# Kernel optimization log

Hardware: AMD Instinct MI355X
Metric: run time of the kernel (lower is better)

Reference implementation:

```python
import jax, jax.numpy as jnp
import numpy as np

N, E, G = 50000, 800000, 128
IN_C, H, EDGE_D, NUM_CLASSES, NUM_LAYERS = 26, 64, 3, 2, 4

def _p(k, shape):
    return jax.random.normal(k, shape, dtype=jnp.float32) * 0.05

def setup_inputs() -> dict:
    key = jax.random.key(0)
    ks = list(jax.random.split(key, 32))
    x = jax.random.normal(ks[0], (N, IN_C), dtype=jnp.float32)
    pos = jax.random.normal(ks[1], (N, 3), dtype=jnp.float32)
    row = jax.random.randint(ks[2], (E,), 0, N, dtype=jnp.int32)
    # avoid self-loops so dist > 0 (norm is non-differentiable at 0)
    off = jax.random.randint(ks[3], (E,), 1, N, dtype=jnp.int32)
    col = (row + off) % N
    edge_index = jnp.stack([row, col], axis=0)
    edge_attr = jax.random.normal(ks[4], (E, EDGE_D), dtype=jnp.float32)
    batch = jnp.sort(jax.random.randint(ks[5], (N,), 0, G, dtype=jnp.int32))
    inp = dict(x=x, pos=pos, edge_index=edge_index, edge_attr=edge_attr, batch=batch)
    inp['proj_W'] = _p(ks[6], (IN_C, H)); inp['proj_b'] = jnp.zeros((H,), jnp.float32)
    inp['msg_W1'] = _p(ks[7], (NUM_LAYERS, 2*H + 1 + EDGE_D, H)); inp['msg_b1'] = jnp.zeros((NUM_LAYERS, H), jnp.float32)
    inp['msg_W2'] = _p(ks[8], (NUM_LAYERS, H, H)); inp['msg_b2'] = jnp.zeros((NUM_LAYERS, H), jnp.float32)
    inp['node_W1'] = _p(ks[9], (NUM_LAYERS, 2*H, H)); inp['node_b1'] = jnp.zeros((NUM_LAYERS, H), jnp.float32)
    inp['node_W2'] = _p(ks[10], (NUM_LAYERS, H, H)); inp['node_b2'] = jnp.zeros((NUM_LAYERS, H), jnp.float32)
    inp['coord_W1'] = _p(ks[11], (NUM_LAYERS - 1, H, H)); inp['coord_b1'] = jnp.zeros((NUM_LAYERS - 1, H), jnp.float32)
    inp['coord_W2'] = _p(ks[12], (NUM_LAYERS - 1, H, 1)); inp['coord_b2'] = jnp.zeros((NUM_LAYERS - 1, 1), jnp.float32)
    inp['cls_W1'] = _p(ks[13], (2*H, H)); inp['cls_b1'] = jnp.zeros((H,), jnp.float32)
    inp['cls_W2'] = _p(ks[14], (H, NUM_CLASSES)); inp['cls_b2'] = jnp.zeros((NUM_CLASSES,), jnp.float32)
    return inp

def _egnn_forward(x, pos, edge_index, edge_attr, batch,
                  proj_W, proj_b, msg_W1, msg_b1, msg_W2, msg_b2,
                  node_W1, node_b1, node_W2, node_b2,
                  coord_W1, coord_b1, coord_W2, coord_b2,
                  cls_W1, cls_b1, cls_W2, cls_b2):
    silu = jax.nn.silu
    row, col = edge_index[0], edge_index[1]
    h = x @ proj_W + proj_b  # [N,H]
    for i in range(NUM_LAYERS):
        diff = pos[row] - pos[col]                      # [E,3]
        dist = jnp.linalg.norm(diff, axis=-1, keepdims=True)  # [E,1]
        msg_in = jnp.concatenate([h[row], h[col], dist, edge_attr], axis=-1)  # [E,2H+1+edge_dim]
        msg = silu(silu(msg_in @ msg_W1[i] + msg_b1[i]) @ msg_W2[i] + msg_b2[i])  # [E,H]
        agg = jax.ops.segment_sum(msg, row, num_segments=N)  # [N,H]
        h_new = silu(jnp.concatenate([h, agg], axis=-1) @ node_W1[i] + node_b1[i]) @ node_W2[i] + node_b2[i]
        h = h + h_new  # residual; dropout is identity at eval
        if i < NUM_LAYERS - 1:
            w = silu(msg @ coord_W1[i] + coord_b1[i]) @ coord_W2[i] + coord_b2[i]  # [E,1]
            pos = pos + jax.ops.segment_sum(diff * w, row, num_segments=N)
    # mean_max pooling over graphs
    sums = jax.ops.segment_sum(h, batch, num_segments=G)
    counts = jax.ops.segment_sum(jnp.ones((h.shape[0],), h.dtype), batch, num_segments=G)
    mean = sums / jnp.maximum(counts, 1.0)[:, None]
    mx = jax.ops.segment_max(h, batch, num_segments=G)
    pooled = jnp.concatenate([mean, mx], axis=-1)  # [G,2H]
    return jax.nn.relu(pooled @ cls_W1 + cls_b1) @ cls_W2 + cls_b2  # [G,num_classes]

def reference(x, pos, edge_index, edge_attr, batch,
              proj_W, proj_b, msg_W1, msg_b1, msg_W2, msg_b2,
              node_W1, node_b1, node_W2, node_b2,
              coord_W1, coord_b1, coord_W2, coord_b2,
              cls_W1, cls_b1, cls_W2, cls_b2):
    return _egnn_forward(x, pos, edge_index, edge_attr, batch,
                         proj_W, proj_b, msg_W1, msg_b1, msg_W2, msg_b2,
                         node_W1, node_b1, node_W2, node_b2,
                         coord_W1, coord_b1, coord_W2, coord_b2,
                         cls_W1, cls_b1, cls_W2, cls_b2)
```

## Files before the change

### kernel.cpp

```cpp
#include <hip/hip_runtime.h>
#include <math.h>


typedef __attribute__((ext_vector_type(8))) short bshort8;
typedef __attribute__((ext_vector_type(4))) float f32x4;
typedef unsigned short ushort;
typedef unsigned int uint;

__device__ __forceinline__ float silu_f(float x)
{
  return x * __builtin_amdgcn_rcpf(1.0f + __expf(-x));
}

__device__ __forceinline__ void bf16_split(float x, ushort& h, ushort& l)
{
  uint bx = __float_as_uint(x);
  ushort hb = (ushort)(bx >> 16);
  float hf = __uint_as_float((uint)hb << 16);
  float r = x - hf;
  l = (ushort)(__float_as_uint(r) >> 16);
  h = hb;
}

#define ROW_FMA(acc, scal, rowptr)                                                   \
  {                                                                                  \
    const float4* _w = (const float4*)(rowptr);                                      \
    _Pragma("unroll") for (int _j = 0; _j < 16; _j++)                                \
    {                                                                                \
      float4 _wv = _w[_j];                                                           \
      acc[4 * _j + 0] += (scal) * _wv.x;                                             \
      acc[4 * _j + 1] += (scal) * _wv.y;                                             \
      acc[4 * _j + 2] += (scal) * _wv.z;                                             \
      acc[4 * _j + 3] += (scal) * _wv.w;                                             \
    }                                                                                \
  }

__global__ __launch_bounds__(256) void proj_kernel(
    const float* __restrict__ x, const float* __restrict__ W, const float* __restrict__ b,
    float* __restrict__ h, int N)
{
  __shared__ float sW[26 * 64];
  __shared__ float sb[64];
  for (int i = threadIdx.x; i < 26 * 64; i += 256) sW[i] = W[i];
  if (threadIdx.x < 64) sb[threadIdx.x] = b[threadIdx.x];
  __syncthreads();
  int n = blockIdx.x * 256 + threadIdx.x;
  if (n >= N) return;
  float acc[64];
#pragma unroll
  for (int j = 0; j < 64; j++) acc[j] = sb[j];
#pragma unroll
  for (int k = 0; k < 26; k++) {
    float xk = x[(size_t)n * 26 + k];
    ROW_FMA(acc, xk, sW + k * 64);
  }
  float4* h4 = (float4*)(h + (size_t)n * 64);
#pragma unroll
  for (int j4 = 0; j4 < 16; j4++) {
    float4 v;
    v.x = acc[4 * j4 + 0]; v.y = acc[4 * j4 + 1]; v.z = acc[4 * j4 + 2]; v.w = acc[4 * j4 + 3];
    h4[j4] = v;
  }
}

#define NB 128
#define ASTR 132

__global__ __launch_bounds__(256) void premul_tiled_kernel(
    const float* __restrict__ h, const float* __restrict__ W1,
    float* __restrict__ P, float* __restrict__ Q, int N)
{
  __shared__ float sA[64 * ASTR];
  __shared__ float sW[64 * 64];
  int t = threadIdx.x;
  int n0 = blockIdx.x * NB;

#pragma unroll
  for (int it = 0; it < 8; it++) {
    int f = t + 256 * it;
    int nl = f >> 4;
    int k4 = f & 15;
    int n = n0 + nl;
    float4 v;
    if (n < N) v = ((const float4*)(h + (size_t)n * 64))[k4];
    else { v.x = v.y = v.z = v.w = 0.f; }
    sA[(4 * k4 + 0) * ASTR + nl] = v.x;
    sA[(4 * k4 + 1) * ASTR + nl] = v.y;
    sA[(4 * k4 + 2) * ASTR + nl] = v.z;
    sA[(4 * k4 + 3) * ASTR + nl] = v.w;
  }
  for (int i = t; i < 4096; i += 256) sW[i] = W1[i];
  __syncthreads();

  int rg = t & 31, cg = t >> 5;
  const float4* sA4 = (const float4*)sA;
  const float4* sW4 = (const float4*)sW;

  float aP[4][8];
#pragma unroll
  for (int i = 0; i < 4; i++)
#pragma unroll
    for (int j = 0; j < 8; j++) aP[i][j] = 0.f;
#pragma unroll 8
  for (int k = 0; k < 64; k++) {
    float4 a = sA4[k * (ASTR / 4) + rg];
    float4 w0 = sW4[k * 16 + 2 * cg];
    float4 w1 = sW4[k * 16 + 2 * cg + 1];
#pragma unroll
    for (int i = 0; i < 4; i++) {
      float av = (i == 0) ? a.x : (i == 1) ? a.y : (i == 2) ? a.z : a.w;
      aP[i][0] += av * w0.x; aP[i][1] += av * w0.y;
      aP[i][2] += av * w0.z; aP[i][3] += av * w0.w;
      aP[i][4] += av * w1.x; aP[i][5] += av * w1.y;
      aP[i][6] += av * w1.z; aP[i][7] += av * w1.w;
    }
  }
  __syncthreads();
  for (int i = t; i < 4096; i += 256) sW[i] = W1[4096 + i];
  __syncthreads();
  float aQ[4][8];
#pragma unroll
  for (int i = 0; i < 4; i++)
#pragma unroll
    for (int j = 0; j < 8; j++) aQ[i][j] = 0.f;
#pragma unroll 8
  for (int k = 0; k < 64; k++) {
    float4 a = sA4[k * (ASTR / 4) + rg];
    float4 w0 = sW4[k * 16 + 2 * cg];
    float4 w1 = sW4[k * 16 + 2 * cg + 1];
#pragma unroll
    for (int i = 0; i < 4; i++) {
      float av = (i == 0) ? a.x : (i == 1) ? a.y : (i == 2) ? a.z : a.w;
      aQ[i][0] += av * w0.x; aQ[i][1] += av * w0.y;
      aQ[i][2] += av * w0.z; aQ[i][3] += av * w0.w;
      aQ[i][4] += av * w1.x; aQ[i][5] += av * w1.y;
      aQ[i][6] += av * w1.z; aQ[i][7] += av * w1.w;
    }
  }
#pragma unroll
  for (int i = 0; i < 4; i++) {
    int n = n0 + 4 * rg + i;
    if (n < N) {
      float4 o0, o1;
      o0.x = aP[i][0]; o0.y = aP[i][1]; o0.z = aP[i][2]; o0.w = aP[i][3];
      o1.x = aP[i][4]; o1.y = aP[i][5]; o1.z = aP[i][6]; o1.w = aP[i][7];
      float4* Pp = (float4*)(P + (size_t)n * 64 + 8 * cg);
      Pp[0] = o0; Pp[1] = o1;
      o0.x = aQ[i][0]; o0.y = aQ[i][1]; o0.z = aQ[i][2]; o0.w = aQ[i][3];
      o1.x = aQ[i][4]; o1.y = aQ[i][5]; o1.z = aQ[i][6]; o1.w = aQ[i][7];
      float4* Qp = (float4*)(Q + (size_t)n * 64 + 8 * cg);
      Qp[0] = o0; Qp[1] = o1;
    }
  }
}

template <int PREMUL>
__global__ __launch_bounds__(256) void node_tiled_kernel(
    float* __restrict__ h, const float* __restrict__ agg,
    const float* __restrict__ W1, const float* __restrict__ b1,
    const float* __restrict__ W2, const float* __restrict__ b2, int N,
    const float* __restrict__ W1n, float* __restrict__ P, float* __restrict__ Q)
{
  __shared__ float sA[64 * ASTR];
  __shared__ float sW[64 * 64];
  __shared__ float sb1v[64], sb2v[64];
  int t = threadIdx.x;
  int n0 = blockIdx.x * NB;
  int rg = t & 31, cg = t >> 5;
  const float4* sA4 = (const float4*)sA;
  const float4* sW4 = (const float4*)sW;

#pragma unroll
  for (int it = 0; it < 8; it++) {
    int f = t + 256 * it;
    int nl = f >> 4;
    int k4 = f & 15;
    int n = n0 + nl;
    float4 v;
    if (n < N) v = ((const float4*)(h + (size_t)n * 64))[k4];
    else { v.x = v.y = v.z = v.w = 0.f; }
    sA[(4 * k4 + 0) * ASTR + nl] = v.x;
    sA[(4 * k4 + 1) * ASTR + nl] = v.y;
    sA[(4 * k4 + 2) * ASTR + nl] = v.z;
    sA[(4 * k4 + 3) * ASTR + nl] = v.w;
  }
  for (int i = t; i < 4096; i += 256) sW[i] = W1[i];
  if (t < 64) { sb1v[t] = b1[t]; sb2v[t] = b2[t]; }
  __syncthreads();

  float u[4][8];
#pragma unroll
  for (int i = 0; i < 4; i++)
#pragma unroll
    for (int j = 0; j < 8; j++) u[i][j] = 0.f;
#pragma unroll 8
  for (int k = 0; k < 64; k++) {
    float4 a = sA4[k * (ASTR / 4) + rg];
    float4 w0 = sW4[k * 16 + 2 * cg];
    float4 w1 = sW4[k * 16 + 2 * cg + 1];
#pragma unroll
    for (int i = 0; i < 4; i++) {
      float av = (i == 0) ? a.x : (i == 1) ? a.y : (i == 2) ? a.z : a.w;
      u[i][0] += av * w0.x; u[i][1] += av * w0.y;
      u[i][2] += av * w0.z; u[i][3] += av * w0.w;
      u[i][4] += av * w1.x; u[i][5] += av * w1.y;
      u[i][6] += av * w1.z; u[i][7] += av * w1.w;
    }
  }
  __syncthreads();

#pragma unroll
  for (int it = 0; it < 8; it++) {
    int f = t + 256 * it;
    int nl = f >> 4;
    int k4 = f & 15;
    int n = n0 + nl;
    float4 v;
    if (n < N) v = ((const float4*)(agg + (size_t)n * 64))[k4];
    else { v.x = v.y = v.z = v.w = 0.f; }
    sA[(4 * k4 + 0) * ASTR + nl] = v.x;
    sA[(4 * k4 + 1) * ASTR + nl] = v.y;
    sA[(4 * k4 + 2) * ASTR + nl] = v.z;
    sA[(4 * k4 + 3) * ASTR + nl] = v.w;
  }
  for (int i = t; i < 4096; i += 256) sW[i] = W1[4096 + i];
  __syncthreads();
#pragma unroll 8
  for (int k = 0; k < 64; k++) {
    float4 a = sA4[k * (ASTR / 4) + rg];
    float4 w0 = sW4[k * 16 + 2 * cg];
    float4 w1 = sW4[k * 16 + 2 * cg + 1];
#pragma unroll
    for (int i = 0; i < 4; i++) {
      float av = (i == 0) ? a.x : (i == 1) ? a.y : (i == 2) ? a.z : a.w;
      u[i][0] += av * w0.x; u[i][1] += av * w0.y;
      u[i][2] += av * w0.z; u[i][3] += av * w0.w;
      u[i][4] += av * w1.x; u[i][5] += av * w1.y;
      u[i][6] += av * w1.z; u[i][7] += av * w1.w;
    }
  }
#pragma unroll
  for (int i = 0; i < 4; i++)
#pragma unroll
    for (int j = 0; j < 8; j++) u[i][j] = silu_f(u[i][j] + sb1v[8 * cg + j]);
  __syncthreads();

#pragma unroll
  for (int j = 0; j < 8; j++)
#pragma unroll
    for (int i = 0; i < 4; i++) sA[(8 * cg + j) * ASTR + (4 * rg + i)] = u[i][j];
  for (int i = t; i < 4096; i += 256) sW[i] = W2[i];
  __syncthreads();

  float o[4][8];
#pragma unroll
  for (int i = 0; i < 4; i++)
#pragma unroll
    for (int j = 0; j < 8; j++) o[i][j] = 0.f;
#pragma unroll 8
  for (int k = 0; k < 64; k++) {
    float4 a = sA4[k * (ASTR / 4) + rg];
    float4 w0 = sW4[k * 16 + 2 * cg];
    float4 w1 = sW4[k * 16 + 2 * cg + 1];
#pragma unroll
    for (int i = 0; i < 4; i++) {
      float av = (i == 0) ? a.x : (i == 1) ? a.y : (i == 2) ? a.z : a.w;
      o[i][0] += av * w0.x; o[i][1] += av * w0.y;
      o[i][2] += av * w0.z; o[i][3] += av * w0.w;
      o[i][4] += av * w1.x; o[i][5] += av * w1.y;
      o[i][6] += av * w1.z; o[i][7] += av * w1.w;
    }
  }
  float hnew[4][8];
#pragma unroll
  for (int i = 0; i < 4; i++) {
    int n = n0 + 4 * rg + i;
    if (n < N) {
      float4* hp = (float4*)(h + (size_t)n * 64 + 8 * cg);
      float4 h0 = hp[0], h1 = hp[1];
      hnew[i][0] = h0.x + o[i][0] + sb2v[8 * cg + 0];
      hnew[i][1] = h0.y + o[i][1] + sb2v[8 * cg + 1];
      hnew[i][2] = h0.z + o[i][2] + sb2v[8 * cg + 2];
      hnew[i][3] = h0.w + o[i][3] + sb2v[8 * cg + 3];
      hnew[i][4] = h1.x + o[i][4] + sb2v[8 * cg + 4];
      hnew[i][5] = h1.y + o[i][5] + sb2v[8 * cg + 5];
      hnew[i][6] = h1.z + o[i][6] + sb2v[8 * cg + 6];
      hnew[i][7] = h1.w + o[i][7] + sb2v[8 * cg + 7];
      float4 s0, s1;
      s0.x = hnew[i][0]; s0.y = hnew[i][1]; s0.z = hnew[i][2]; s0.w = hnew[i][3];
      s1.x = hnew[i][4]; s1.y = hnew[i][5]; s1.z = hnew[i][6]; s1.w = hnew[i][7];
      hp[0] = s0; hp[1] = s1;
    } else {
#pragma unroll
      for (int j = 0; j < 8; j++) hnew[i][j] = 0.f;
    }
  }

  if (PREMUL) {
    __syncthreads();
#pragma unroll
    for (int j = 0; j < 8; j++)
#pragma unroll
      for (int i = 0; i < 4; i++) sA[(8 * cg + j) * ASTR + (4 * rg + i)] = hnew[i][j];
    for (int i = t; i < 4096; i += 256) sW[i] = W1n[i];
    __syncthreads();
    float aP[4][8];
#pragma unroll
    for (int i = 0; i < 4; i++)
#pragma unroll
      for (int j = 0; j < 8; j++) aP[i][j] = 0.f;
#pragma unroll 8
    for (int k = 0; k < 64; k++) {
      float4 a = sA4[k * (ASTR / 4) + rg];
      float4 w0 = sW4[k * 16 + 2 * cg];
      float4 w1 = sW4[k * 16 + 2 * cg + 1];
#pragma unroll
      for (int i = 0; i < 4; i++) {
        float av = (i == 0) ? a.x : (i == 1) ? a.y : (i == 2) ? a.z : a.w;
        aP[i][0] += av * w0.x; aP[i][1] += av * w0.y;
        aP[i][2] += av * w0.z; aP[i][3] += av * w0.w;
        aP[i][4] += av * w1.x; aP[i][5] += av * w1.y;
        aP[i][6] += av * w1.z; aP[i][7] += av * w1.w;
      }
    }
#pragma unroll
    for (int i = 0; i < 4; i++) {
      int n = n0 + 4 * rg + i;
      if (n < N) {
        float4 o0, o1;
        o0.x = aP[i][0]; o0.y = aP[i][1]; o0.z = aP[i][2]; o0.w = aP[i][3];
        o1.x = aP[i][4]; o1.y = aP[i][5]; o1.z = aP[i][6]; o1.w = aP[i][7];
        float4* Pp = (float4*)(P + (size_t)n * 64 + 8 * cg);
        Pp[0] = o0; Pp[1] = o1;
      }
    }
    __syncthreads();
    for (int i = t; i < 4096; i += 256) sW[i] = W1n[4096 + i];
    __syncthreads();
    float aQ[4][8];
#pragma unroll
    for (int i = 0; i < 4; i++)
#pragma unroll
      for (int j = 0; j < 8; j++) aQ[i][j] = 0.f;
#pragma unroll 8
    for (int k = 0; k < 64; k++) {
      float4 a = sA4[k * (ASTR / 4) + rg];
      float4 w0 = sW4[k * 16 + 2 * cg];
      float4 w1 = sW4[k * 16 + 2 * cg + 1];
#pragma unroll
      for (int i = 0; i < 4; i++) {
        float av = (i == 0) ? a.x : (i == 1) ? a.y : (i == 2) ? a.z : a.w;
        aQ[i][0] += av * w0.x; aQ[i][1] += av * w0.y;
        aQ[i][2] += av * w0.z; aQ[i][3] += av * w0.w;
        aQ[i][4] += av * w1.x; aQ[i][5] += av * w1.y;
        aQ[i][6] += av * w1.z; aQ[i][7] += av * w1.w;
      }
    }
#pragma unroll
    for (int i = 0; i < 4; i++) {
      int n = n0 + 4 * rg + i;
      if (n < N) {
        float4 o0, o1;
        o0.x = aQ[i][0]; o0.y = aQ[i][1]; o0.z = aQ[i][2]; o0.w = aQ[i][3];
        o1.x = aQ[i][4]; o1.y = aQ[i][5]; o1.z = aQ[i][6]; o1.w = aQ[i][7];
        float4* Qp = (float4*)(Q + (size_t)n * 64 + 8 * cg);
        Qp[0] = o0; Qp[1] = o1;
      }
    }
  }
}

__global__ __launch_bounds__(256) void hist_kernel(
    const int* __restrict__ row, int* __restrict__ cnt, int E)
{
  int e = blockIdx.x * 256 + threadIdx.x;
  if (e < E) atomicAdd(&cnt[row[e]], 1);
}

__global__ __launch_bounds__(1024) void scan_kernel(
    const int* __restrict__ cnt, int* __restrict__ rowptr, int* __restrict__ cursor, int N, int E)
{
  __shared__ int part[1024];
  int t = threadIdx.x;
  int chunk = (N + 1023) >> 10;
  int lo = t * chunk;
  int hi = lo + chunk;
  if (lo > N) lo = N;
  if (hi > N) hi = N;
  int s = 0;
  for (int i = lo; i < hi; i++) s += cnt[i];
  part[t] = s;
  __syncthreads();
  for (int off = 1; off < 1024; off <<= 1) {
    int v = 0;
    if (t >= off) v = part[t - off];
    __syncthreads();
    if (t >= off) part[t] += v;
    __syncthreads();
  }
  int run = part[t] - s;
  for (int i = lo; i < hi; i++) {
    rowptr[i] = run;
    cursor[i] = run;
    run += cnt[i];
  }
  if (t == 0) rowptr[N] = E;
}

__global__ __launch_bounds__(256) void scatter_kernel(
    const int* __restrict__ row, const int* __restrict__ col, const float* __restrict__ eattr,
    int* __restrict__ cursor, int* __restrict__ srow, int* __restrict__ scol,
    float* __restrict__ sea4, int E)
{
  int e = blockIdx.x * 256 + threadIdx.x;
  if (e >= E) return;
  int r = row[e];
  int p = atomicAdd(&cursor[r], 1);
  srow[p] = r;
  scol[p] = col[e];
  float4 v;
  v.x = eattr[(size_t)e * 3 + 0];
  v.y = eattr[(size_t)e * 3 + 1];
  v.z = eattr[(size_t)e * 3 + 2];
  v.w = 0.f;
  ((float4*)sea4)[p] = v;
}

__global__ __launch_bounds__(256) void prep_wt_kernel(
    const float* __restrict__ W2all, const float* __restrict__ C1all,
    ushort* __restrict__ w2h, ushort* __restrict__ w2l,
    ushort* __restrict__ c1h, ushort* __restrict__ c1l)
{
  int idx = blockIdx.x * 256 + threadIdx.x;
  if (idx >= 4 * 4096) return;
  int layer = idx >> 12, rem = idx & 4095;
  int k = rem >> 6, c = rem & 63;
  int oidx = layer * 4096 + c * 64 + k;
  ushort h, l;
  bf16_split(W2all[idx], h, l);
  w2h[oidx] = h; w2l[oidx] = l;
  if (layer < 3) {
    bf16_split(C1all[idx], h, l);
    c1h[oidx] = h; c1l[oidx] = l;
  }
}

#define EB 128

__device__ __forceinline__ bshort8 lds_frag(const ushort* base, int edge, int kb)
{
  int byte = edge * 128 + kb * 2;
  byte ^= (edge & 7) << 4;
  return *(const bshort8*)((const char*)base + byte);
}

template <int COORD>
__global__ __launch_bounds__(256) void edge_fused_kernel(
    const int* __restrict__ srow, const int* __restrict__ scol, const int* __restrict__ rowptr,
    const float* __restrict__ posr, float* __restrict__ posw,
    const float* __restrict__ sea4,
    const float* __restrict__ P, const float* __restrict__ Q,
    const float* __restrict__ W1t, const float* __restrict__ b1,
    const ushort* __restrict__ w2h, const ushort* __restrict__ w2l,
    const float* __restrict__ b2,
    const ushort* __restrict__ c1h, const ushort* __restrict__ c1l,
    const float* __restrict__ cb1, const float* __restrict__ cW2,
    const float* __restrict__ cb2,
    float* __restrict__ agg, int E)
{
  __shared__ ushort sUhi[EB * 64];
  __shared__ ushort sUlo[EB * 64];
  __shared__ float sW1t[4 * 64];
  __shared__ float sb1v[64], sb2v[64];
  __shared__ float sDiff[3][EB];
  __shared__ float sWe[EB];
  __shared__ int sShare[COORD ? EB * 4 : EB];
  __shared__ float scb1v[COORD ? 64 : 1];
  __shared__ float scW2v[COORD ? 64 : 1];
  __shared__ int sSlotCnt[2];
  __shared__ int sSlotStart[EB + 2];
  __shared__ int sSlotRowF[EB];

  int* s_srow = sShare;
  float* sPart = (float*)sShare;

  int t = threadIdx.x;
  sW1t[t] = W1t[t];
  if (t < 64) { sb1v[t] = b1[t]; sb2v[t] = b2[t]; }
  if (COORD && t >= 64 && t < 128) { scb1v[t - 64] = cb1[t - 64]; scW2v[t - 64] = cW2[t - 64]; }
  __syncthreads();

  int e0 = blockIdx.x * EB;
  int nE = E - e0; if (nE > EB) nE = EB;

#pragma unroll
  for (int p = 0; p < 4; p++) {
    int eloc = p * 32 + (t >> 3);
    int ks = t & 7;
    int e = e0 + eloc;
    int base = eloc * 128 + ks * 16;
    int swz = (eloc & 7) << 4;
    if (e < E) {
      int r = srow[e];
      int c = scol[e];
      float prx = posr[(size_t)r * 3 + 0], pry = posr[(size_t)r * 3 + 1],
            prz = posr[(size_t)r * 3 + 2];
      float pcx = posr[(size_t)c * 3 + 0], pcy = posr[(size_t)c * 3 + 1],
            pcz = posr[(size_t)c * 3 + 2];
      float dx = prx - pcx, dy = pry - pcy, dz = prz - pcz;
      float dist = sqrtf(dx * dx + dy * dy + dz * dz);
      if (ks == 0) {
        s_srow[eloc] = r;
        sDiff[0][eloc] = dx; sDiff[1][eloc] = dy; sDiff[2][eloc] = dz;
      }
      float4 ea = ((const float4*)sea4)[e];
      const float4* P4p = (const float4*)(P + (size_t)r * 64) + ks * 2;
      const float4* Q4p = (const float4*)(Q + (size_t)c * 64) + ks * 2;
      float4 a0 = P4p[0], a1 = P4p[1];
      float4 q0 = Q4p[0], q1 = Q4p[1];
      float pa[8] = {a0.x, a0.y, a0.z, a0.w, a1.x, a1.y, a1.z, a1.w};
      float qa[8] = {q0.x, q0.y, q0.z, q0.w, q1.x, q1.y, q1.z, q1.w};
      ushort hh[8], ll[8];
#pragma unroll
      for (int kk = 0; kk < 8; kk++) {
        int k = ks * 8 + kk;
        float val = pa[kk] + qa[kk] + sb1v[k] + dist * sW1t[k] + ea.x * sW1t[64 + k] +
                    ea.y * sW1t[128 + k] + ea.z * sW1t[192 + k];
        float uv = silu_f(val);
        bf16_split(uv, hh[kk], ll[kk]);
      }
      uint4 hv, lv;
      hv.x = (uint)hh[0] | ((uint)hh[1] << 16);
      hv.y = (uint)hh[2] | ((uint)hh[3] << 16);
      hv.z = (uint)hh[4] | ((uint)hh[5] << 16);
      hv.w = (uint)hh[6] | ((uint)hh[7] << 16);
      lv.x = (uint)ll[0] | ((uint)ll[1] << 16);
// ... 198 lines not shown
  ssum[grp][j] = s;
  smax[grp][j] = mx;
  __syncthreads();
  if (grp == 0) {
    float S = ssum[0][j] + ssum[1][j] + ssum[2][j] + ssum[3][j];
    float M = fmaxf(fmaxf(smax[0][j], smax[1][j]), fmaxf(smax[2][j], smax[3][j]));
    float cnt = (float)(end - start);
    pooled[j] = S / fmaxf(cnt, 1.0f);
    pooled[64 + j] = M;
  }
  __syncthreads();
  if (threadIdx.x < 64) {
    float a = b1[j];
#pragma unroll
    for (int k = 0; k < 128; k++) a += pooled[k] * W1[k * 64 + j];
    su[j] = fmaxf(a, 0.f);
  }
  __syncthreads();
  if (threadIdx.x < 2) {
    float a = b2[threadIdx.x];
#pragma unroll
    for (int k = 0; k < 64; k++) a += su[k] * W2[k * 2 + threadIdx.x];
    out[g * 2 + threadIdx.x] = a;
  }
}

extern "C" void kernel_launch(void* const* d_in, const int* in_sizes, int n_in,
                              void* d_out, int out_size, void* d_ws, size_t ws_size,
                              hipStream_t stream)
{
  const float* x = (const float*)d_in[0];
  const float* pos = (const float*)d_in[1];
  const int* ei = (const int*)d_in[2];
  const float* eattr = (const float*)d_in[3];
  const int* batch = (const int*)d_in[4];
  const float* projW = (const float*)d_in[5];
  const float* projb = (const float*)d_in[6];
  const float* msgW1 = (const float*)d_in[7];
  const float* msgb1 = (const float*)d_in[8];
  const float* msgW2 = (const float*)d_in[9];
  const float* msgb2 = (const float*)d_in[10];
  const float* ndW1 = (const float*)d_in[11];
  const float* ndb1 = (const float*)d_in[12];
  const float* ndW2 = (const float*)d_in[13];
  const float* ndb2 = (const float*)d_in[14];
  const float* cdW1 = (const float*)d_in[15];
  const float* cdb1 = (const float*)d_in[16];
  const float* cdW2 = (const float*)d_in[17];
  const float* cdb2 = (const float*)d_in[18];
  const float* clsW1 = (const float*)d_in[19];
  const float* clsb1 = (const float*)d_in[20];
  const float* clsW2 = (const float*)d_in[21];
  const float* clsb2 = (const float*)d_in[22];

  int N = in_sizes[4];
  int E = in_sizes[3] / 3;
  const int* rowp = ei;
  const int* colp = ei + E;

  char* wsb = (char*)d_ws;
  size_t off = 0;
  auto alloc = [&](size_t bytes) {
    size_t o = off;
    off = (off + bytes + 255) & ~(size_t)255;
    return o;
  };
  size_t nh = (size_t)N * 64 * sizeof(float);
  size_t o_h = alloc(nh);
  size_t o_P = alloc(nh);
  size_t o_Q = alloc(nh);
  size_t o_agg = alloc(nh);
  size_t o_posA = alloc((size_t)N * 3 * sizeof(float));
  size_t o_posB = alloc((size_t)N * 3 * sizeof(float));
  size_t o_cnt = alloc((size_t)N * sizeof(int));
  size_t o_rowptr = alloc(((size_t)N + 1) * sizeof(int));
  size_t o_cursor = alloc((size_t)N * sizeof(int));
  size_t o_srow = alloc((size_t)E * sizeof(int));
  size_t o_scol = alloc((size_t)E * sizeof(int));
  size_t o_sea4 = alloc((size_t)E * 4 * sizeof(float));
  size_t o_w2h = alloc(4 * 4096 * sizeof(ushort));
  size_t o_w2l = alloc(4 * 4096 * sizeof(ushort));
  size_t o_c1h = alloc(4 * 4096 * sizeof(ushort));
  size_t o_c1l = alloc(4 * 4096 * sizeof(ushort));
  size_t csr_end = off;

  float* h = (float*)(wsb + o_h);
  float* Pb = (float*)(wsb + o_P);
  float* Qb = (float*)(wsb + o_Q);
  float* agg = (float*)(wsb + o_agg);
  float* posA = (float*)(wsb + o_posA);
  float* posB = (float*)(wsb + o_posB);

  int nb_nodes = (N + 255) / 256;
  int nb_edges = (E + 255) / 256;
  int nb_tiled = (N + NB - 1) / NB;
  int G = out_size / 2;

  proj_kernel<<<nb_nodes, 256, 0, stream>>>(x, projW, projb, h, N);

  const float* pr[4] = {pos, posA, posB, posA};
  float* pw[4] = {posA, posB, posA, nullptr};

  bool use_sorted = (csr_end <= ws_size);

  if (use_sorted) {
    int* cnt = (int*)(wsb + o_cnt);
    int* rowptr = (int*)(wsb + o_rowptr);
    int* cursor = (int*)(wsb + o_cursor);
    int* srow = (int*)(wsb + o_srow);
    int* scol = (int*)(wsb + o_scol);
    float* sea4 = (float*)(wsb + o_sea4);
    ushort* w2h = (ushort*)(wsb + o_w2h);
    ushort* w2l = (ushort*)(wsb + o_w2l);
    ushort* c1h = (ushort*)(wsb + o_c1h);
    ushort* c1l = (ushort*)(wsb + o_c1l);

    hipMemsetAsync(cnt, 0, (size_t)N * sizeof(int), stream);
    hist_kernel<<<nb_edges, 256, 0, stream>>>(rowp, cnt, E);
    scan_kernel<<<1, 1024, 0, stream>>>(cnt, rowptr, cursor, N, E);
    scatter_kernel<<<nb_edges, 256, 0, stream>>>(rowp, colp, eattr, cursor, srow, scol, sea4, E);
    prep_wt_kernel<<<64, 256, 0, stream>>>(msgW2, cdW1, w2h, w2l, c1h, c1l);

    premul_tiled_kernel<<<nb_tiled, 256, 0, stream>>>(h, msgW1, Pb, Qb, N);

    int nb_fused = (E + EB - 1) / EB;
    for (int i = 0; i < 4; i++) {
      hipMemsetAsync(agg, 0, nh, stream);
      if (i < 3) {
        hipMemcpyAsync(pw[i], pr[i], (size_t)N * 3 * sizeof(float), hipMemcpyDeviceToDevice,
                       stream);
        edge_fused_kernel<1><<<nb_fused, 256, 0, stream>>>(
            srow, scol, rowptr, pr[i], pw[i], sea4, Pb, Qb,
            msgW1 + (size_t)i * 132 * 64 + 128 * 64, msgb1 + i * 64,
            w2h + (size_t)i * 4096, w2l + (size_t)i * 4096, msgb2 + i * 64,
            c1h + (size_t)i * 4096, c1l + (size_t)i * 4096,
            cdb1 + i * 64, cdW2 + i * 64, cdb2 + i, agg, E);
        node_tiled_kernel<1><<<nb_tiled, 256, 0, stream>>>(
            h, agg, ndW1 + (size_t)i * 8192, ndb1 + i * 64, ndW2 + (size_t)i * 4096,
            ndb2 + i * 64, N, msgW1 + (size_t)(i + 1) * 132 * 64, Pb, Qb);
      } else {
        edge_fused_kernel<0><<<nb_fused, 256, 0, stream>>>(
            srow, scol, rowptr, pr[i], nullptr, sea4, Pb, Qb,
            msgW1 + (size_t)i * 132 * 64 + 128 * 64, msgb1 + i * 64,
            w2h + (size_t)i * 4096, w2l + (size_t)i * 4096, msgb2 + i * 64,
            nullptr, nullptr, nullptr, nullptr, nullptr, agg, E);
        node_tiled_kernel<0><<<nb_tiled, 256, 0, stream>>>(
            h, agg, ndW1 + (size_t)i * 8192, ndb1 + i * 64, ndW2 + (size_t)i * 4096,
            ndb2 + i * 64, N, nullptr, nullptr, nullptr);
      }
    }
  } else {
    for (int i = 0; i < 4; i++) {
      premul_tiled_kernel<<<nb_tiled, 256, 0, stream>>>(h, msgW1 + (size_t)i * 132 * 64, Pb, Qb,
                                                        N);
      hipMemsetAsync(agg, 0, nh, stream);
      node_tiled_kernel<0><<<nb_tiled, 256, 0, stream>>>(
          h, agg, ndW1 + (size_t)i * 8192, ndb1 + i * 64, ndW2 + (size_t)i * 4096, ndb2 + i * 64,
          N, nullptr, nullptr, nullptr);
    }
  }

  pool_cls_kernel<<<G, 256, 0, stream>>>(h, batch, N, clsW1, clsb1, clsW2, clsb2, (float*)d_out);
}
```

Baseline: 913.7 us.

## Move node MLP and premul GEMMs onto bf16x3 MFMA with presplit weights

Replaces the FP32 FMA-tiled node-update and P/Q premultiply kernels with MFMA kernels. These use a three-product bf16 hi/lo split to keep near-fp32 accuracy. A new prep kernel pre-splits and transposes the node and msgW1 weights into bf16 hi/lo buffers once per call, and activations are staged into swizzled LDS as hi/lo bf16. The aim is to cut the ALU time of the per-node GEMMs, at the cost of extra split work and slightly lower precision. It also removes the fallback path used when the workspace is too small, so that case now does no message passing.

```diff
diff --git a/kernel.cpp b/kernel.cpp
--- a/kernel.cpp
+++ b/kernel.cpp
@@ -63,308 +63,265 @@
   }
 }
 
-#define NB 128
-#define ASTR 132
-
-__global__ __launch_bounds__(256) void premul_tiled_kernel(
-    const float* __restrict__ h, const float* __restrict__ W1,
+#define EB 128
+
+__device__ __forceinline__ bshort8 lds_frag(const ushort* base, int edge, int kb)
+{
+  int byte = edge * 128 + kb * 2;
+  byte ^= (edge & 7) << 4;
+  return *(const bshort8*)((const char*)base + byte);
+}
+
+__device__ __forceinline__ void stage_tile_f32(
+    const float* __restrict__ src, int n0, int N, ushort* sHi, ushort* sLo, int t)
+{
+#pragma unroll
+  for (int p = 0; p < 4; p++) {
+    int nl = p * 32 + (t >> 3);
+    int ks = t & 7;
+    int n = n0 + nl;
+    int base = nl * 128 + ks * 16;
+    int swz = (nl & 7) << 4;
+    if (n < N) {
+      const float4* sp = (const float4*)(src + (size_t)n * 64) + ks * 2;
+      float4 a0 = sp[0], a1 = sp[1];
+      float va[8] = {a0.x, a0.y, a0.z, a0.w, a1.x, a1.y, a1.z, a1.w};
+      ushort hh[8], ll[8];
+#pragma unroll
+      for (int kk = 0; kk < 8; kk++) bf16_split(va[kk], hh[kk], ll[kk]);
+      uint4 hv, lv;
+      hv.x = (uint)hh[0] | ((uint)hh[1] << 16);
+      hv.y = (uint)hh[2] | ((uint)hh[3] << 16);
+      hv.z = (uint)hh[4] | ((uint)hh[5] << 16);
+      hv.w = (uint)hh[6] | ((uint)hh[7] << 16);
+      lv.x = (uint)ll[0] | ((uint)ll[1] << 16);
+      lv.y = (uint)ll[2] | ((uint)ll[3] << 16);
+      lv.z = (uint)ll[4] | ((uint)ll[5] << 16);
+      lv.w = (uint)ll[6] | ((uint)ll[7] << 16);
+      *(uint4*)((char*)sHi + (base ^ swz)) = hv;
+      *(uint4*)((char*)sLo + (base ^ swz)) = lv;
+    } else {
+      uint4 z; z.x = 0; z.y = 0; z.z = 0; z.w = 0;
+      *(uint4*)((char*)sHi + (base ^ swz)) = z;
+      *(uint4*)((char*)sLo + (base ^ swz)) = z;
+    }
+  }
+}
+
+#define PANEL_MFMA(accv, bhp, blp, sHi, sLo)                                         \
+  {                                                                                  \
+    bshort8 wh0 = *(const bshort8*)(bhp);                                            \
+    bshort8 wh1 = *(const bshort8*)((bhp) + 32);                                     \
+    bshort8 wl0 = *(const bshort8*)(blp);                                            \
+    bshort8 wl1 = *(const bshort8*)((blp) + 32);                                     \
+    _Pragma("unroll") for (int et = 0; et < 8; et++)                                 \
+    {                                                                                \
+      int nd = et * 16 + lane16;                                                     \
+      bshort8 ah0 = lds_frag(sHi, nd, kq * 8);                                       \
+      bshort8 ah1 = lds_frag(sHi, nd, 32 + kq * 8);                                  \
+      bshort8 al0 = lds_frag(sLo, nd, kq * 8);                                       \
+      bshort8 al1 = lds_frag(sLo, nd, 32 + kq * 8);                                  \
+      f32x4 a = accv[et];                                                            \
+      a = __builtin_amdgcn_mfma_f32_16x16x32_bf16(wh0, ah0, a, 0, 0, 0);             \
+      a = __builtin_amdgcn_mfma_f32_16x16x32_bf16(wh1, ah1, a, 0, 0, 0);             \
+      a = __builtin_amdgcn_mfma_f32_16x16x32_bf16(wh0, al0, a, 0, 0, 0);             \
+      a = __builtin_amdgcn_mfma_f32_16x16x32_bf16(wh1, al1, a, 0, 0, 0);             \
+      a = __builtin_amdgcn_mfma_f32_16x16x32_bf16(wl0, ah0, a, 0, 0, 0);             \
+      a = __builtin_amdgcn_mfma_f32_16x16x32_bf16(wl1, ah1, a, 0, 0, 0);             \
+      accv[et] = a;                                                                  \
+    }                                                                                \
+  }
+
+__global__ __launch_bounds__(256) void premul_mfma_kernel(
+    const float* __restrict__ h, const ushort* __restrict__ pqh, const ushort* __restrict__ pql,
     float* __restrict__ P, float* __restrict__ Q, int N)
 {
-  __shared__ float sA[64 * ASTR];
-  __shared__ float sW[64 * 64];
+  __shared__ ushort sAhi[EB * 64];
+  __shared__ ushort sAlo[EB * 64];
   int t = threadIdx.x;
-  int n0 = blockIdx.x * NB;
-
-#pragma unroll
-  for (int it = 0; it < 8; it++) {
-    int f = t + 256 * it;
-    int nl = f >> 4;
-    int k4 = f & 15;
-    int n = n0 + nl;
-    float4 v;
-    if (n < N) v = ((const float4*)(h + (size_t)n * 64))[k4];
-    else { v.x = v.y = v.z = v.w = 0.f; }
-    sA[(4 * k4 + 0) * ASTR + nl] = v.x;
-    sA[(4 * k4 + 1) * ASTR + nl] = v.y;
-    sA[(4 * k4 + 2) * ASTR + nl] = v.z;
-    sA[(4 * k4 + 3) * ASTR + nl] = v.w;
-  }
-  for (int i = t; i < 4096; i += 256) sW[i] = W1[i];
-  __syncthreads();
-
-  int rg = t & 31, cg = t >> 5;
-  const float4* sA4 = (const float4*)sA;
-  const float4* sW4 = (const float4*)sW;
-
-  float aP[4][8];
-#pragma unroll
-  for (int i = 0; i < 4; i++)
-#pragma unroll
-    for (int j = 0; j < 8; j++) aP[i][j] = 0.f;
-#pragma unroll 8
-  for (int k = 0; k < 64; k++) {
-    float4 a = sA4[k * (ASTR / 4) + rg];
-    float4 w0 = sW4[k * 16 + 2 * cg];
-    float4 w1 = sW4[k * 16 + 2 * cg + 1];
-#pragma unroll
-    for (int i = 0; i < 4; i++) {
-      float av = (i == 0) ? a.x : (i == 1) ? a.y : (i == 2) ? a.z : a.w;
-      aP[i][0] += av * w0.x; aP[i][1] += av * w0.y;
-      aP[i][2] += av * w0.z; aP[i][3] += av * w0.w;
-      aP[i][4] += av * w1.x; aP[i][5] += av * w1.y;
-      aP[i][6] += av * w1.z; aP[i][7] += av * w1.w;
-    }
-  }
-  __syncthreads();
-  for (int i = t; i < 4096; i += 256) sW[i] = W1[4096 + i];
-  __syncthreads();
-  float aQ[4][8];
-#pragma unroll
-  for (int i = 0; i < 4; i++)
-#pragma unroll
-    for (int j = 0; j < 8; j++) aQ[i][j] = 0.f;
-#pragma unroll 8
-  for (int k = 0; k < 64; k++) {
-    float4 a = sA4[k * (ASTR / 4) + rg];
-    float4 w0 = sW4[k * 16 + 2 * cg];
-    float4 w1 = sW4[k * 16 + 2 * cg + 1];
-#pragma unroll
-    for (int i = 0; i < 4; i++) {
-      float av = (i == 0) ? a.x : (i == 1) ? a.y : (i == 2) ? a.z : a.w;
-      aQ[i][0] += av * w0.x; aQ[i][1] += av * w0.y;
-      aQ[i][2] += av * w0.z; aQ[i][3] += av * w0.w;
-      aQ[i][4] += av * w1.x; aQ[i][5] += av * w1.y;
-      aQ[i][6] += av * w1.z; aQ[i][7] += av * w1.w;
-    }
-  }
-#pragma unroll
-  for (int i = 0; i < 4; i++) {
-    int n = n0 + 4 * rg + i;
+  int n0 = blockIdx.x * EB;
+  stage_tile_f32(h, n0, N, sAhi, sAlo, t);
+  __syncthreads();
+
+  int l = t & 63, wv = t >> 6, lane16 = l & 15, kq = l >> 4;
+  int col = wv * 16 + kq * 4;
+
+  f32x4 acc[8];
+#pragma unroll
+  for (int et = 0; et < 8; et++) { f32x4 z = {0.f, 0.f, 0.f, 0.f}; acc[et] = z; }
+  {
+    const ushort* bh = pqh + (wv * 16 + lane16) * 64 + kq * 8;
+    const ushort* bl = pql + (wv * 16 + lane16) * 64 + kq * 8;
+    PANEL_MFMA(acc, bh, bl, sAhi, sAlo);
+  }
+#pragma unroll
+  for (int et = 0; et < 8; et++) {
+    int n = n0 + et * 16 + lane16;
     if (n < N) {
-      float4 o0, o1;
-      o0.x = aP[i][0]; o0.y = aP[i][1]; o0.z = aP[i][2]; o0.w = aP[i][3];
-      o1.x = aP[i][4]; o1.y = aP[i][5]; o1.z = aP[i][6]; o1.w = aP[i][7];
-      float4* Pp = (float4*)(P + (size_t)n * 64 + 8 * cg);
-      Pp[0] = o0; Pp[1] = o1;
-      o0.x = aQ[i][0]; o0.y = aQ[i][1]; o0.z = aQ[i][2]; o0.w = aQ[i][3];
-      o1.x = aQ[i][4]; o1.y = aQ[i][5]; o1.z = aQ[i][6]; o1.w = aQ[i][7];
-      float4* Qp = (float4*)(Q + (size_t)n * 64 + 8 * cg);
-      Qp[0] = o0; Qp[1] = o1;
+      float4 v; v.x = acc[et][0]; v.y = acc[et][1]; v.z = acc[et][2]; v.w = acc[et][3];
+      *(float4*)(P + (size_t)n * 64 + col) = v;
+    }
+  }
+#pragma unroll
+  for (int et = 0; et < 8; et++) { f32x4 z = {0.f, 0.f, 0.f, 0.f}; acc[et] = z; }
+  {
+    const ushort* bh = pqh + 4096 + (wv * 16 + lane16) * 64 + kq * 8;
+    const ushort* bl = pql + 4096 + (wv * 16 + lane16) * 64 + kq * 8;
+    PANEL_MFMA(acc, bh, bl, sAhi, sAlo);
+  }
+#pragma unroll
+  for (int et = 0; et < 8; et++) {
+    int n = n0 + et * 16 + lane16;
+    if (n < N) {
+      float4 v; v.x = acc[et][0]; v.y = acc[et][1]; v.z = acc[et][2]; v.w = acc[et][3];
+      *(float4*)(Q + (size_t)n * 64 + col) = v;
     }
   }
 }
 
 template <int PREMUL>
-__global__ __launch_bounds__(256) void node_tiled_kernel(
+__global__ __launch_bounds__(256) void node_mfma_kernel(
     float* __restrict__ h, const float* __restrict__ agg,
-    const float* __restrict__ W1, const float* __restrict__ b1,
-    const float* __restrict__ W2, const float* __restrict__ b2, int N,
-    const float* __restrict__ W1n, float* __restrict__ P, float* __restrict__ Q)
-{
-  __shared__ float sA[64 * ASTR];
-  __shared__ float sW[64 * 64];
+    const ushort* __restrict__ n1h, const ushort* __restrict__ n1l,
+    const float* __restrict__ b1,
+    const ushort* __restrict__ n2h, const ushort* __restrict__ n2l,
+    const float* __restrict__ b2,
+    const ushort* __restrict__ pqh, const ushort* __restrict__ pql,
+    float* __restrict__ P, float* __restrict__ Q, int N)
+{
+  __shared__ ushort sAhi[EB * 64];
+  __shared__ ushort sAlo[EB * 64];
   __shared__ float sb1v[64], sb2v[64];
   int t = threadIdx.x;
-  int n0 = blockIdx.x * NB;
-  int rg = t & 31, cg = t >> 5;
-  const float4* sA4 = (const float4*)sA;
-  const float4* sW4 = (const float4*)sW;
-
-#pragma unroll
-  for (int it = 0; it < 8; it++) {
-    int f = t + 256 * it;
-    int nl = f >> 4;
-    int k4 = f & 15;
-    int n = n0 + nl;
-    float4 v;
-    if (n < N) v = ((const float4*)(h + (size_t)n * 64))[k4];
-    else { v.x = v.y = v.z = v.w = 0.f; }
-    sA[(4 * k4 + 0) * ASTR + nl] = v.x;
-    sA[(4 * k4 + 1) * ASTR + nl] = v.y;
-    sA[(4 * k4 + 2) * ASTR + nl] = v.z;
-    sA[(4 * k4 + 3) * ASTR + nl] = v.w;
-  }
-  for (int i = t; i < 4096; i += 256) sW[i] = W1[i];
+  int n0 = blockIdx.x * EB;
   if (t < 64) { sb1v[t] = b1[t]; sb2v[t] = b2[t]; }
-  __syncthreads();
-
-  float u[4][8];
-#pragma unroll
-  for (int i = 0; i < 4; i++)
-#pragma unroll
-    for (int j = 0; j < 8; j++) u[i][j] = 0.f;
-#pragma unroll 8
-  for (int k = 0; k < 64; k++) {
-    float4 a = sA4[k * (ASTR / 4) + rg];
-    float4 w0 = sW4[k * 16 + 2 * cg];
-    float4 w1 = sW4[k * 16 + 2 * cg + 1];
-#pragma unroll
-    for (int i = 0; i < 4; i++) {
-      float av = (i == 0) ? a.x : (i == 1) ? a.y : (i == 2) ? a.z : a.w;
-      u[i][0] += av * w0.x; u[i][1] += av * w0.y;
-      u[i][2] += av * w0.z; u[i][3] += av * w0.w;
-      u[i][4] += av * w1.x; u[i][5] += av * w1.y;
-      u[i][6] += av * w1.z; u[i][7] += av * w1.w;
-    }
-  }
-  __syncthreads();
-
-#pragma unroll
-  for (int it = 0; it < 8; it++) {
-    int f = t + 256 * it;
-    int nl = f >> 4;
-    int k4 = f & 15;
-    int n = n0 + nl;
-    float4 v;
-    if (n < N) v = ((const float4*)(agg + (size_t)n * 64))[k4];
-    else { v.x = v.y = v.z = v.w = 0.f; }
-    sA[(4 * k4 + 0) * ASTR + nl] = v.x;
-    sA[(4 * k4 + 1) * ASTR + nl] = v.y;
-    sA[(4 * k4 + 2) * ASTR + nl] = v.z;
-    sA[(4 * k4 + 3) * ASTR + nl] = v.w;
-  }
-  for (int i = t; i < 4096; i += 256) sW[i] = W1[4096 + i];
-  __syncthreads();
-#pragma unroll 8
-  for (int k = 0; k < 64; k++) {
-    float4 a = sA4[k * (ASTR / 4) + rg];
-    float4 w0 = sW4[k * 16 + 2 * cg];
-    float4 w1 = sW4[k * 16 + 2 * cg + 1];
-#pragma unroll
-    for (int i = 0; i < 4; i++) {
-      float av = (i == 0) ? a.x : (i == 1) ? a.y : (i == 2) ? a.z : a.w;
-      u[i][0] += av * w0.x; u[i][1] += av * w0.y;
-      u[i][2] += av * w0.z; u[i][3] += av * w0.w;
-      u[i][4] += av * w1.x; u[i][5] += av * w1.y;
-      u[i][6] += av * w1.z; u[i][7] += av * w1.w;
-    }
-  }
-#pragma unroll
-  for (int i = 0; i < 4; i++)
-#pragma unroll
-    for (int j = 0; j < 8; j++) u[i][j] = silu_f(u[i][j] + sb1v[8 * cg + j]);
-  __syncthreads();
-
-#pragma unroll
-  for (int j = 0; j < 8; j++)
-#pragma unroll
-    for (int i = 0; i < 4; i++) sA[(8 * cg + j) * ASTR + (4 * rg + i)] = u[i][j];
-  for (int i = t; i < 4096; i += 256) sW[i] = W2[i];
-  __syncthreads();
-
-  float o[4][8];
-#pragma unroll
-  for (int i = 0; i < 4; i++)
-#pragma unroll
-    for (int j = 0; j < 8; j++) o[i][j] = 0.f;
-#pragma unroll 8
-  for (int k = 0; k < 64; k++) {
-    float4 a = sA4[k * (ASTR / 4) + rg];
-    float4 w0 = sW4[k * 16 + 2 * cg];
-    float4 w1 = sW4[k * 16 + 2 * cg + 1];
-#pragma unroll
-    for (int i = 0; i < 4; i++) {
-      float av = (i == 0) ? a.x : (i == 1) ? a.y : (i == 2) ? a.z : a.w;
-      o[i][0] += av * w0.x; o[i][1] += av * w0.y;
-      o[i][2] += av * w0.z; o[i][3] += av * w0.w;
-      o[i][4] += av * w1.x; o[i][5] += av * w1.y;
-      o[i][6] += av * w1.z; o[i][7] += av * w1.w;
-    }
-  }
-  float hnew[4][8];
-#pragma unroll
-  for (int i = 0; i < 4; i++) {
-    int n = n0 + 4 * rg + i;
-    if (n < N) {
-      float4* hp = (float4*)(h + (size_t)n * 64 + 8 * cg);
-      float4 h0 = hp[0], h1 = hp[1];
-      hnew[i][0] = h0.x + o[i][0] + sb2v[8 * cg + 0];
-      hnew[i][1] = h0.y + o[i][1] + sb2v[8 * cg + 1];
-      hnew[i][2] = h0.z + o[i][2] + sb2v[8 * cg + 2];
-      hnew[i][3] = h0.w + o[i][3] + sb2v[8 * cg + 3];
-      hnew[i][4] = h1.x + o[i][4] + sb2v[8 * cg + 4];
-      hnew[i][5] = h1.y + o[i][5] + sb2v[8 * cg + 5];
-      hnew[i][6] = h1.z + o[i][6] + sb2v[8 * cg + 6];
-      hnew[i][7] = h1.w + o[i][7] + sb2v[8 * cg + 7];
-      float4 s0, s1;
-      s0.x = hnew[i][0]; s0.y = hnew[i][1]; s0.z = hnew[i][2]; s0.w = hnew[i][3];
-      s1.x = hnew[i][4]; s1.y = hnew[i][5]; s1.z = hnew[i][6]; s1.w = hnew[i][7];
-      hp[0] = s0; hp[1] = s1;
-    } else {
-#pragma unroll
-      for (int j = 0; j < 8; j++) hnew[i][j] = 0.f;
+
+  stage_tile_f32(h, n0, N, sAhi, sAlo, t);
+  __syncthreads();
+
+  int l = t & 63, wv = t >> 6, lane16 = l & 15, kq = l >> 4;
+  int col = wv * 16 + kq * 4;
+
+  f32x4 acc[8];
+#pragma unroll
+  for (int et = 0; et < 8; et++) { f32x4 z = {0.f, 0.f, 0.f, 0.f}; acc[et] = z; }
+  {
+    const ushort* bh = n1h + (wv * 16 + lane16) * 128 + kq * 8;
+    const ushort* bl = n1l + (wv * 16 + lane16) * 128 + kq * 8;
+    PANEL_MFMA(acc, bh, bl, sAhi, sAlo);
+  }
+  __syncthreads();
+  stage_tile_f32(agg, n0, N, sAhi, sAlo, t);
+  __syncthreads();
+  {
+    const ushort* bh = n1h + (wv * 16 + lane16) * 128 + 64 + kq * 8;
+    const ushort* bl = n1l + (wv * 16 + lane16) * 128 + 64 + kq * 8;
+    PANEL_MFMA(acc, bh, bl, sAhi, sAlo);
+  }
+  __syncthreads();
+
+  {
+    float b1r[4];
+#pragma unroll
+    for (int r = 0; r < 4; r++) b1r[r] = sb1v[col + r];
+#pragma unroll
+    for (int et = 0; et < 8; et++) {
+      int nd = et * 16 + lane16;
+      ushort uh[4], ul[4];
+#pragma unroll
+      for (int r = 0; r < 4; r++) {
+        float uv = silu_f(acc[et][r] + b1r[r]);
+        bf16_split(uv, uh[r], ul[r]);
+      }
+      int byte = (nd * 128 + col * 2) ^ ((nd & 7) << 4);
+      uint2 hv, lv;
+      hv.x = (uint)uh[0] | ((uint)uh[1] << 16);
+      hv.y = (uint)uh[2] | ((uint)uh[3] << 16);
+      lv.x = (uint)ul[0] | ((uint)ul[1] << 16);
+      lv.y = (uint)ul[2] | ((uint)ul[3] << 16);
+      *(uint2*)((char*)sAhi + byte) = hv;
+      *(uint2*)((char*)sAlo + byte) = lv;
+    }
+  }
+  __syncthreads();
+
+#pragma unroll
+  for (int et = 0; et < 8; et++) { f32x4 z = {0.f, 0.f, 0.f, 0.f}; acc[et] = z; }
+  {
+    const ushort* bh = n2h + (wv * 16 + lane16) * 64 + kq * 8;
+    const ushort* bl = n2l + (wv * 16 + lane16) * 64 + kq * 8;
+    PANEL_MFMA(acc, bh, bl, sAhi, sAlo);
+  }
+  uint2 hnh[8], hnl[8];
+  {
+    float b2r[4];
+#pragma unroll
+    for (int r = 0; r < 4; r++) b2r[r] = sb2v[col + r];
+#pragma unroll
+    for (int et = 0; et < 8; et++) {
+      int n = n0 + et * 16 + lane16;
+      float hn[4];
+      if (n < N) {
+        float4 hv = *(float4*)(h + (size_t)n * 64 + col);
+        hn[0] = hv.x + acc[et][0] + b2r[0];
+        hn[1] = hv.y + acc[et][1] + b2r[1];
+        hn[2] = hv.z + acc[et][2] + b2r[2];
+        hn[3] = hv.w + acc[et][3] + b2r[3];
+        float4 sv; sv.x = hn[0]; sv.y = hn[1]; sv.z = hn[2]; sv.w = hn[3];
+        *(float4*)(h + (size_t)n * 64 + col) = sv;
+      } else {
+        hn[0] = hn[1] = hn[2] = hn[3] = 0.f;
+      }
+      if (PREMUL) {
+        ushort sh[4], sl[4];
+#pragma unroll
+        for (int r = 0; r < 4; r++) bf16_split(hn[r], sh[r], sl[r]);
+        hnh[et].x = (uint)sh[0] | ((uint)sh[1] << 16);
+        hnh[et].y = (uint)sh[2] | ((uint)sh[3] << 16);
+        hnl[et].x = (uint)sl[0] | ((uint)sl[1] << 16);
+        hnl[et].y = (uint)sl[2] | ((uint)sl[3] << 16);
+      }
     }
   }
 
   if (PREMUL) {
     __syncthreads();
 #pragma unroll
-    for (int j = 0; j < 8; j++)
-#pragma unroll
-      for (int i = 0; i < 4; i++) sA[(8 * cg + j) * ASTR + (4 * rg + i)] = hnew[i][j];
-    for (int i = t; i < 4096; i += 256) sW[i] = W1n[i];
+    for (int et = 0; et < 8; et++) {
+      int nd = et * 16 + lane16;
+      int byte = (nd * 128 + col * 2) ^ ((nd & 7) << 4);
+      *(uint2*)((char*)sAhi + byte) = hnh[et];
+      *(uint2*)((char*)sAlo + byte) = hnl[et];
+    }
     __syncthreads();
-    float aP[4][8];
-#pragma unroll
-    for (int i = 0; i < 4; i++)
-#pragma unroll
-      for (int j = 0; j < 8; j++) aP[i][j] = 0.f;
-#pragma unroll 8
-    for (int k = 0; k < 64; k++) {
-      float4 a = sA4[k * (ASTR / 4) + rg];
-      float4 w0 = sW4[k * 16 + 2 * cg];
-      float4 w1 = sW4[k * 16 + 2 * cg + 1];
-#pragma unroll
-      for (int i = 0; i < 4; i++) {
-        float av = (i == 0) ? a.x : (i == 1) ? a.y : (i == 2) ? a.z : a.w;
-        aP[i][0] += av * w0.x; aP[i][1] += av * w0.y;
-        aP[i][2] += av * w0.z; aP[i][3] += av * w0.w;
-        aP[i][4] += av * w1.x; aP[i][5] += av * w1.y;
-        aP[i][6] += av * w1.z; aP[i][7] += av * w1.w;
-      }
-    }
-#pragma unroll
-    for (int i = 0; i < 4; i++) {
-      int n = n0 + 4 * rg + i;
+#pragma unroll
+    for (int et = 0; et < 8; et++) { f32x4 z = {0.f, 0.f, 0.f, 0.f}; acc[et] = z; }
+    {
+      const ushort* bh = pqh + (wv * 16 + lane16) * 64 + kq * 8;
+      const ushort* bl = pql + (wv * 16 + lane16) * 64 + kq * 8;
+      PANEL_MFMA(acc, bh, bl, sAhi, sAlo);
+    }
+#pragma unroll
+    for (int et = 0; et < 8; et++) {
+      int n = n0 + et * 16 + lane16;
       if (n < N) {
-        float4 o0, o1;
-        o0.x = aP[i][0]; o0.y = aP[i][1]; o0.z = aP[i][2]; o0.w = aP[i][3];
-        o1.x = aP[i][4]; o1.y = aP[i][5]; o1.z = aP[i][6]; o1.w = aP[i][7];
-        float4* Pp = (float4*)(P + (size_t)n * 64 + 8 * cg);
-        Pp[0] = o0; Pp[1] = o1;
-      }
-    }
-    __syncthreads();
-    for (int i = t; i < 4096; i += 256) sW[i] = W1n[4096 + i];
-    __syncthreads();
-    float aQ[4][8];
-#pragma unroll
-    for (int i = 0; i < 4; i++)
-#pragma unroll
-      for (int j = 0; j < 8; j++) aQ[i][j] = 0.f;
-#pragma unroll 8
-    for (int k = 0; k < 64; k++) {
-      float4 a = sA4[k * (ASTR / 4) + rg];
-      float4 w0 = sW4[k * 16 + 2 * cg];
-      float4 w1 = sW4[k * 16 + 2 * cg + 1];
-#pragma unroll
-      for (int i = 0; i < 4; i++) {
-        float av = (i == 0) ? a.x : (i == 1) ? a.y : (i == 2) ? a.z : a.w;
-        aQ[i][0] += av * w0.x; aQ[i][1] += av * w0.y;
-        aQ[i][2] += av * w0.z; aQ[i][3] += av * w0.w;
-        aQ[i][4] += av * w1.x; aQ[i][5] += av * w1.y;
-        aQ[i][6] += av * w1.z; aQ[i][7] += av * w1.w;
-      }
-    }
-#pragma unroll
-    for (int i = 0; i < 4; i++) {
-      int n = n0 + 4 * rg + i;
+        float4 v; v.x = acc[et][0]; v.y = acc[et][1]; v.z = acc[et][2]; v.w = acc[et][3];
+        *(float4*)(P + (size_t)n * 64 + col) = v;
+      }
+    }
+#pragma unroll
+    for (int et = 0; et < 8; et++) { f32x4 z = {0.f, 0.f, 0.f, 0.f}; acc[et] = z; }
+    {
+      const ushort* bh = pqh + 4096 + (wv * 16 + lane16) * 64 + kq * 8;
+      const ushort* bl = pql + 4096 + (wv * 16 + lane16) * 64 + kq * 8;
+      PANEL_MFMA(acc, bh, bl, sAhi, sAlo);
+    }
+#pragma unroll
+    for (int et = 0; et < 8; et++) {
+      int n = n0 + et * 16 + lane16;
       if (n < N) {
-        float4 o0, o1;
-        o0.x = aQ[i][0]; o0.y = aQ[i][1]; o0.z = aQ[i][2]; o0.w = aQ[i][3];
-        o1.x = aQ[i][4]; o1.y = aQ[i][5]; o1.z = aQ[i][6]; o1.w = aQ[i][7];
-        float4* Qp = (float4*)(Q + (size_t)n * 64 + 8 * cg);
-        Qp[0] = o0; Qp[1] = o1;
+        float4 v; v.x = acc[et][0]; v.y = acc[et][1]; v.z = acc[et][2]; v.w = acc[et][3];
+        *(float4*)(Q + (size_t)n * 64 + col) = v;
       }
     }
   }
@@ -445,13 +402,38 @@
   }
 }
 
-#define EB 128
-
-__device__ __forceinline__ bshort8 lds_frag(const ushort* base, int edge, int kb)
-{
-  int byte = edge * 128 + kb * 2;
-  byte ^= (edge & 7) << 4;
-  return *(const bshort8*)((const char*)base + byte);
+__global__ __launch_bounds__(256) void prep_nd_kernel(
+    const float* __restrict__ ndW1, const float* __restrict__ ndW2,
+    const float* __restrict__ msgW1,
+    ushort* __restrict__ n1h, ushort* __restrict__ n1l,
+    ushort* __restrict__ n2h, ushort* __restrict__ n2l,
+    ushort* __restrict__ pqh, ushort* __restrict__ pql)
+{
+  int idx = blockIdx.x * 256 + threadIdx.x;
+  if (idx < 4 * 8192) {
+    int i = idx >> 13, rem = idx & 8191;
+    int k = rem >> 6, c = rem & 63;
+    ushort h, l;
+    bf16_split(ndW1[idx], h, l);
+    int o = i * 8192 + c * 128 + k;
+    n1h[o] = h; n1l[o] = l;
+  }
+  if (idx < 4 * 4096) {
+    int i = idx >> 12, rem = idx & 4095;
+    int k = rem >> 6, c = rem & 63;
+    ushort h, l;
+    bf16_split(ndW2[idx], h, l);
+    int o = i * 4096 + c * 64 + k;
+    n2h[o] = h; n2l[o] = l;
+  }
+  if (idx < 4 * 8192) {
+    int i = idx >> 13, rem = idx & 8191;
+    int k = rem >> 6, c = rem & 63;
+    ushort h, l;
+    bf16_split(msgW1[(size_t)i * 132 * 64 + k * 64 + c], h, l);
+    int o = i * 8192 + (k >> 6) * 4096 + c * 64 + (k & 63);
+    pqh[o] = h; pql[o] = l;
+  }
 }
 
 template <int COORD>
@@ -816,6 +798,12 @@
   size_t o_w2l = alloc(4 * 4096 * sizeof(ushort));
   size_t o_c1h = alloc(4 * 4096 * sizeof(ushort));
   size_t o_c1l = alloc(4 * 4096 * sizeof(ushort));
+  size_t o_n1h = alloc(4 * 8192 * sizeof(ushort));
+  size_t o_n1l = alloc(4 * 8192 * sizeof(ushort));
+  size_t o_n2h = alloc(4 * 4096 * sizeof(ushort));
+  size_t o_n2l = alloc(4 * 4096 * sizeof(ushort));
+  size_t o_pqh = alloc(4 * 8192 * sizeof(ushort));
+  size_t o_pql = alloc(4 * 8192 * sizeof(ushort));
   size_t csr_end = off;
 
   float* h = (float*)(wsb + o_h);
@@ -827,7 +815,7 @@
 
   int nb_nodes = (N + 255) / 256;
   int nb_edges = (E + 255) / 256;
-  int nb_tiled = (N + NB - 1) / NB;
+  int nb_tiled = (N + EB - 1) / EB;
   int G = out_size / 2;
 
   proj_kernel<<<nb_nodes, 256, 0, stream>>>(x, projW, projb, h, N);
@@ -848,14 +836,21 @@
     ushort* w2l = (ushort*)(wsb + o_w2l);
     ushort* c1h = (ushort*)(wsb + o_c1h);
     ushort* c1l = (ushort*)(wsb + o_c1l);
+    ushort* n1h = (ushort*)(wsb + o_n1h);
+    ushort* n1l = (ushort*)(wsb + o_n1l);
+    ushort* n2h = (ushort*)(wsb + o_n2h);
+    ushort* n2l = (ushort*)(wsb + o_n2l);
+    ushort* pqh = (ushort*)(wsb + o_pqh);
+    ushort* pql = (ushort*)(wsb + o_pql);
 
     hipMemsetAsync(cnt, 0, (size_t)N * sizeof(int), stream);
     hist_kernel<<<nb_edges, 256, 0, stream>>>(rowp, cnt, E);
     scan_kernel<<<1, 1024, 0, stream>>>(cnt, rowptr, cursor, N, E);
     scatter_kernel<<<nb_edges, 256, 0, stream>>>(rowp, colp, eattr, cursor, srow, scol, sea4, E);
     prep_wt_kernel<<<64, 256, 0, stream>>>(msgW2, cdW1, w2h, w2l, c1h, c1l);
-
-    premul_tiled_kernel<<<nb_tiled, 256, 0, stream>>>(h, msgW1, Pb, Qb, N);
+    prep_nd_kernel<<<128, 256, 0, stream>>>(ndW1, ndW2, msgW1, n1h, n1l, n2h, n2l, pqh, pql);
+
+    premul_mfma_kernel<<<nb_tiled, 256, 0, stream>>>(h, pqh, pql, Pb, Qb, N);
 
     int nb_fused = (E + EB - 1) / EB;
     for (int i = 0; i < 4; i++) {
@@ -869,28 +864,21 @@
             w2h + (size_t)i * 4096, w2l + (size_t)i * 4096, msgb2 + i * 64,
             c1h + (size_t)i * 4096, c1l + (size_t)i * 4096,
             cdb1 + i * 64, cdW2 + i * 64, cdb2 + i, agg, E);
-        node_tiled_kernel<1><<<nb_tiled, 256, 0, stream>>>(
-            h, agg, ndW1 + (size_t)i * 8192, ndb1 + i * 64, ndW2 + (size_t)i * 4096,
-            ndb2 + i * 64, N, msgW1 + (size_t)(i + 1) * 132 * 64, Pb, Qb);
+        node_mfma_kernel<1><<<nb_tiled, 256, 0, stream>>>(
+            h, agg, n1h + (size_t)i * 8192, n1l + (size_t)i * 8192, ndb1 + i * 64,
+            n2h + (size_t)i * 4096, n2l + (size_t)i * 4096, ndb2 + i * 64,
+            pqh + (size_t)(i + 1) * 8192, pql + (size_t)(i + 1) * 8192, Pb, Qb, N);
       } else {
         edge_fused_kernel<0><<<nb_fused, 256, 0, stream>>>(
             srow, scol, rowptr, pr[i], nullptr, sea4, Pb, Qb,
             msgW1 + (size_t)i * 132 * 64 + 128 * 64, msgb1 + i * 64,
             w2h + (size_t)i * 4096, w2l + (size_t)i * 4096, msgb2 + i * 64,
             nullptr, nullptr, nullptr, nullptr, nullptr, agg, E);
-        node_tiled_kernel<0><<<nb_tiled, 256, 0, stream>>>(
-            h, agg, ndW1 + (size_t)i * 8192, ndb1 + i * 64, ndW2 + (size_t)i * 4096,
-            ndb2 + i * 64, N, nullptr, nullptr, nullptr);
-      }
-    }
-  } else {
-    for (int i = 0; i < 4; i++) {
-      premul_tiled_kernel<<<nb_tiled, 256, 0, stream>>>(h, msgW1 + (size_t)i * 132 * 64, Pb, Qb,
-                                                        N);
-      hipMemsetAsync(agg, 0, nh, stream);
-      node_tiled_kernel<0><<<nb_tiled, 256, 0, stream>>>(
-          h, agg, ndW1 + (size_t)i * 8192, ndb1 + i * 64, ndW2 + (size_t)i * 4096, ndb2 + i * 64,
-          N, nullptr, nullptr, nullptr);
+        node_mfma_kernel<0><<<nb_tiled, 256, 0, stream>>>(
+            h, agg, n1h + (size_t)i * 8192, n1l + (size_t)i * 8192, ndb1 + i * 64,
+            n2h + (size_t)i * 4096, n2l + (size_t)i * 4096, ndb2 + i * 64,
+            nullptr, nullptr, nullptr, nullptr, N);
+      }
     }
   }
 
```

New measurement: 796.1 us (median of 2 runs). 1.15x faster.
